# Kernel tuning notes

Measured on AMD Instinct MI355X. Metric: run time of the kernel, lower is better.

## Reference

```python
import jax, jax.numpy as jnp
import numpy as np

DIM = 1024
N_HEADS = 16
HEAD_DIM = DIM // N_HEADS
LN_EPS = 1e-5


def layer_norm(x, gamma, beta):
    mu = jnp.mean(x, axis=-1, keepdims=True)
    var = jnp.var(x, axis=-1, keepdims=True)
    return (x - mu) * jax.lax.rsqrt(var + LN_EPS) * gamma + beta


def setup_inputs() -> dict:
    key = jax.random.key(0)
    ks = jax.random.split(key, 12)
    B, Nq, Nc, D = 2, 2048, 2048, DIM
    s = 1.0 / np.sqrt(D)
    return {
        "query": jax.random.normal(ks[0], (B, Nq, D), jnp.float32),
        "context": jax.random.normal(ks[1], (B, Nc, D), jnp.float32),
        "Wq": jax.random.normal(ks[2], (D, D), jnp.float32) * s,
        "bq": jnp.zeros((D,), jnp.float32),
        "Wk": jax.random.normal(ks[3], (D, D), jnp.float32) * s,
        "bk": jnp.zeros((D,), jnp.float32),
        "Wv": jax.random.normal(ks[4], (D, D), jnp.float32) * s,
        "bv": jnp.zeros((D,), jnp.float32),
        "Wo": jax.random.normal(ks[5], (D, D), jnp.float32) * s,
        "bo": jnp.zeros((D,), jnp.float32),
        "gq": jnp.ones((D,), jnp.float32),
        "betaq": jnp.zeros((D,), jnp.float32),
        "gkv": jnp.ones((D,), jnp.float32),
        "betakv": jnp.zeros((D,), jnp.float32),
    }


def reference(query, context, Wq, bq, Wk, bk, Wv, bv, Wo, bo, gq, betaq, gkv, betakv):
    B, Nq, D = query.shape
    Nc = context.shape[1]
    residual = query
    q = layer_norm(query, gq, betaq)
    c = layer_norm(context, gkv, betakv)
    # projections; (B,N,D) -> (B,H,N,hd)
    Q = (q @ Wq + bq).reshape(B, Nq, N_HEADS, HEAD_DIM).transpose(0, 2, 1, 3)
    K = (c @ Wk + bk).reshape(B, Nc, N_HEADS, HEAD_DIM).transpose(0, 2, 1, 3)
    V = (c @ Wv + bv).reshape(B, Nc, N_HEADS, HEAD_DIM).transpose(0, 2, 1, 3)
    scores = jnp.einsum("bhqd,bhkd->bhqk", Q, K) / np.sqrt(HEAD_DIM).astype(np.float32)
    attn = jax.nn.softmax(scores, axis=-1)
    out = jnp.einsum("bhqk,bhkd->bhqd", attn, V)
    out = out.transpose(0, 2, 1, 3).reshape(B, Nq, D)
    return residual + out @ Wo + bo
```

## Files before the change

kernel.cpp:

```cpp
#include <hip/hip_runtime.h>
#include <hip/hip_bf16.h>

typedef unsigned short u16;
typedef unsigned long long u64;
typedef __bf16 bf16x8 __attribute__((ext_vector_type(8)));
typedef float f32x4 __attribute__((ext_vector_type(4)));

#define DIM 1024
#define NH 16
#define HD 64
#define QSCALE 0.180336880972788f

__device__ __forceinline__ u16 f2bf(float f) {
  union { float f; unsigned u; } v; v.f = f;
  unsigned r = v.u + 0x7fffu + ((v.u >> 16) & 1u);
  return (u16)(r >> 16);
}

__device__ __forceinline__ unsigned pk2(float a, float b) {
  union { __hip_bfloat162 h; unsigned u; } cv;
  cv.h = __float22bfloat162_rn(make_float2(a, b));
  return cv.u;
}

__device__ __forceinline__ float bf2f(unsigned s) {
  union { unsigned u; float f; } v; v.u = s << 16; return v.f;
}

__device__ __forceinline__ void gld16(const u16* gp, u16* lp) {
  __builtin_amdgcn_global_load_lds(
      (const __attribute__((address_space(1))) unsigned int*)(const void*)gp,
      (__attribute__((address_space(3))) unsigned int*)(void*)lp, 16, 0, 0);
}

__global__ __launch_bounds__(256) void prep_kernel(
    const float* __restrict__ q, const float* __restrict__ c,
    const float* __restrict__ gq, const float* __restrict__ bq,
    const float* __restrict__ gkv, const float* __restrict__ bkv,
    u16* __restrict__ qn, u16* __restrict__ cn,
    const float* W0, const float* W1, const float* W2, const float* W3,
    u16* O0, u16* O1, u16* O2, u16* O3) {
  __shared__ float red[2][4];
  __shared__ float t[32][33];
  int bid = blockIdx.x, tid = threadIdx.x;
  if (bid < 8192) {
    const float* x  = bid < 4096 ? q : c;
    const float* g  = bid < 4096 ? gq : gkv;
    const float* be = bid < 4096 ? bq : bkv;
    u16* out = bid < 4096 ? qn : cn;
    int row = bid & 4095;
    float4 v = ((const float4*)(x + (size_t)row * DIM))[tid];
    float s1 = v.x + v.y + v.z + v.w;
    float s2 = v.x * v.x + v.y * v.y + v.z * v.z + v.w * v.w;
#pragma unroll
    for (int o = 32; o >= 1; o >>= 1) { s1 += __shfl_xor(s1, o, 64); s2 += __shfl_xor(s2, o, 64); }
    int wv = tid >> 6;
    if ((tid & 63) == 0) { red[0][wv] = s1; red[1][wv] = s2; }
    __syncthreads();
    s1 = red[0][0] + red[0][1] + red[0][2] + red[0][3];
    s2 = red[1][0] + red[1][1] + red[1][2] + red[1][3];
    float mu = s1 * (1.f / DIM);
    float var = s2 * (1.f / DIM) - mu * mu;
    float rs = rsqrtf(var + 1e-5f);
    float4 gv = ((const float4*)g)[tid];
    float4 bv = ((const float4*)be)[tid];
    uint2 o2;
    o2.x = pk2((v.x - mu) * rs * gv.x + bv.x, (v.y - mu) * rs * gv.y + bv.y);
    o2.y = pk2((v.z - mu) * rs * gv.z + bv.z, (v.w - mu) * rs * gv.w + bv.w);
    ((uint2*)(out + (size_t)row * DIM))[tid] = o2;
  } else {
    int wid = bid - 8192;
    int z = wid >> 10;
    const float* W = z == 0 ? W0 : z == 1 ? W1 : z == 2 ? W2 : W3;
    u16* O        = z == 0 ? O0 : z == 1 ? O1 : z == 2 ? O2 : O3;
    int xy = wid & 1023;
    int bx = (xy & 31) * 32, by = (xy >> 5) * 32;
    int tx = tid & 31, ty = tid >> 5;
#pragma unroll
    for (int i = 0; i < 4; ++i) t[ty + i * 8][tx] = W[(size_t)(by + ty + i * 8) * DIM + bx + tx];
    __syncthreads();
#pragma unroll
    for (int i = 0; i < 4; ++i) O[(size_t)(bx + ty + i * 8) * DIM + by + tx] = f2bf(t[tx][ty + i * 8]);
  }
}

struct GArg { const u16* A; const u16* Bt; const float* bias; void* out; int mode; };
struct GArg3 { GArg g[3]; };

__global__ __launch_bounds__(256) void gemm128(GArg3 args) {
  GArg ga = args.g[blockIdx.z];
  const u16* __restrict__ A  = ga.A;
  const u16* __restrict__ Bt = ga.Bt;
  __shared__ __align__(16) u16 sm[128 * 64 * 2];
  u16* As = sm;
  u16* Bs = sm + 128 * 64;
  int tid = threadIdx.x, wave = tid >> 6, lane = tid & 63;
  int lr = lane & 15, quad = lane >> 4;
  int m0 = blockIdx.x * 128, n0 = blockIdx.y * 128;
  int wm = (wave >> 1) * 64, wn = (wave & 1) * 64;
  f32x4 acc[4][4] = {};
  for (int kt = 0; kt < DIM; kt += 64) {
#pragma unroll
    for (int r = 0; r < 4; ++r) {
      int slot = tid + r * 256;
      int row = slot >> 3;
      int c = (slot & 7) ^ (row & 7);
      gld16(A + (size_t)(m0 + row) * DIM + kt + c * 8, &As[slot * 8]);
    }
#pragma unroll
    for (int r = 0; r < 4; ++r) {
      int slot = tid + r * 256;
      int row = slot >> 3;
      int c = (slot & 7) ^ (row & 7);
      gld16(Bt + (size_t)(n0 + row) * DIM + kt + c * 8, &Bs[slot * 8]);
    }
    __syncthreads();
#pragma unroll
    for (int kc = 0; kc < 2; ++kc) {
      int pc = ((kc * 4 + quad) ^ (lr & 7)) * 8;
      bf16x8 af[4], bfr[4];
#pragma unroll
      for (int i = 0; i < 4; ++i) {
        af[i]  = *(const bf16x8*)&As[(wm + i * 16 + lr) * 64 + pc];
        bfr[i] = *(const bf16x8*)&Bs[(wn + i * 16 + lr) * 64 + pc];
      }
#pragma unroll
      for (int mi = 0; mi < 4; ++mi)
#pragma unroll
        for (int ni = 0; ni < 4; ++ni)
          acc[mi][ni] = __builtin_amdgcn_mfma_f32_16x16x32_bf16(af[mi], bfr[ni], acc[mi][ni], 0, 0, 0);
    }
    __syncthreads();
  }
  int mode = ga.mode;
  const float* bias = ga.bias;
#pragma unroll
  for (int mi = 0; mi < 4; ++mi)
#pragma unroll
    for (int ni = 0; ni < 4; ++ni) {
      int col = n0 + wn + ni * 16 + lr;
      float bv = bias[col];
      int row0 = m0 + wm + mi * 16 + quad * 4;
      if (mode == 2) {
        int bb = row0 >> 11, t0 = row0 & 2047;
        u64 pk = 0;
#pragma unroll
        for (int r = 0; r < 4; ++r)
          pk |= (u64)f2bf(acc[mi][ni][r] + bv) << (16 * r);
        *(u64*)&((u16*)ga.out)[((size_t)(bb << 10) + col) * 2048 + t0] = pk;
      } else {
        float sc = (mode == 1) ? QSCALE : 1.f;
#pragma unroll
        for (int r = 0; r < 4; ++r)
          ((u16*)ga.out)[(size_t)(row0 + r) * DIM + col] = f2bf((acc[mi][ni][r] + bv) * sc);
      }
    }
}

__global__ __launch_bounds__(256) void gemm_o(const u16* __restrict__ A,
    const u16* __restrict__ Bt, const float* __restrict__ bias,
    float* __restrict__ out, const float* __restrict__ resid) {
  __shared__ __align__(16) u16 sm[(128 + 64) * 64];
  u16* As = sm;
  u16* Bs = sm + 128 * 64;
  int tid = threadIdx.x, wave = tid >> 6, lane = tid & 63;
  int lr = lane & 15, quad = lane >> 4;
  int m0 = blockIdx.x * 128, n0 = blockIdx.y * 64;
  int wm = (wave >> 1) * 64, wn = (wave & 1) * 32;
  f32x4 acc[4][2] = {};
  for (int kt = 0; kt < DIM; kt += 64) {
#pragma unroll
    for (int r = 0; r < 4; ++r) {
      int slot = tid + r * 256;
      int row = slot >> 3;
      int c = (slot & 7) ^ (row & 7);
      gld16(A + (size_t)(m0 + row) * DIM + kt + c * 8, &As[slot * 8]);
    }
#pragma unroll
    for (int r = 0; r < 2; ++r) {
      int slot = tid + r * 256;
      int row = slot >> 3;
      int c = (slot & 7) ^ (row & 7);
      gld16(Bt + (size_t)(n0 + row) * DIM + kt + c * 8, &Bs[slot * 8]);
    }
    __syncthreads();
#pragma unroll
    for (int kc = 0; kc < 2; ++kc) {
      int pc = ((kc * 4 + quad) ^ (lr & 7)) * 8;
      bf16x8 af[4], bfr[2];
#pragma unroll
      for (int i = 0; i < 4; ++i) af[i] = *(const bf16x8*)&As[(wm + i * 16 + lr) * 64 + pc];
#pragma unroll
      for (int j = 0; j < 2; ++j) bfr[j] = *(const bf16x8*)&Bs[(wn + j * 16 + lr) * 64 + pc];
#pragma unroll
      for (int mi = 0; mi < 4; ++mi)
#pragma unroll
        for (int ni = 0; ni < 2; ++ni)
          acc[mi][ni] = __builtin_amdgcn_mfma_f32_16x16x32_bf16(af[mi], bfr[ni], acc[mi][ni], 0, 0, 0);
    }
    __syncthreads();
  }
#pragma unroll
  for (int mi = 0; mi < 4; ++mi)
#pragma unroll
    for (int ni = 0; ni < 2; ++ni) {
      int col = n0 + wn + ni * 16 + lr;
      float bv = bias[col];
      int row0 = m0 + wm + mi * 16 + quad * 4;
#pragma unroll
      for (int r = 0; r < 4; ++r) {
        int row = row0 + r;
        out[(size_t)row * DIM + col] = acc[mi][ni][r] + bv + resid[(size_t)row * DIM + col];
      }
    }
}

#define FK0 0
#define FV0 4096
#define FK1 8192
#define FV1 12288
#define FQP 16384
__global__ __launch_bounds__(256) void flash_kernel(const u16* __restrict__ Q,
    const u16* __restrict__ Kg, const u16* __restrict__ Vt,
    u16* __restrict__ O0, u16* __restrict__ O1,
    float* __restrict__ L0, float* __restrict__ L1) {
  __shared__ __align__(16) u16 lds[24576];
  int tid = threadIdx.x, wave = tid >> 6, lane = tid & 63;
  int lr = lane & 15, quad = lane >> 4;
  int bh = blockIdx.x, b = bh >> 4, h = bh & 15;
  int q0 = blockIdx.y * 128;
  int split = blockIdx.z;
  u16* Op = split ? O1 : O0;
  float* Lp = split ? L1 : L0;
  int t0 = split * 1024;

  const u16* qbase = Q + (size_t)(b * 2048 + q0) * DIM + h * HD;
  const u16* kbase = Kg + (size_t)(b * 2048 + t0) * DIM + h * HD;
  const u16* vbase = Vt + (size_t)(b * 1024 + h * HD) * 2048 + t0;

#pragma unroll
  for (int r = 0; r < 4; ++r) {
    int slot = tid + r * 256;
    int row = slot >> 3;
    int c = (slot & 7) ^ (row & 7);
    gld16(qbase + (size_t)row * DIM + c * 8, &lds[FQP + slot * 8]);
  }
#pragma unroll
  for (int r = 0; r < 2; ++r) {
    int slot = tid + r * 256;
    int row = slot >> 3;
    int c = (slot & 7) ^ (row & 7);
    gld16(kbase + (size_t)row * DIM + c * 8, &lds[FK0 + slot * 8]);
    gld16(vbase + (size_t)row * 2048 + c * 8, &lds[FV0 + slot * 8]);
  }
  __syncthreads();

  bf16x8 qf[2][2];
#pragma unroll
  for (int s = 0; s < 2; ++s)
#pragma unroll
    for (int kc = 0; kc < 2; ++kc)
      qf[s][kc] = *(const bf16x8*)&lds[FQP + (wave * 32 + s * 16 + lr) * 64 +
                                       (((kc * 4 + quad) ^ (lr & 7)) * 8)];

  int pb = FQP + wave * 2048;
  float plsum[2] = {0.f, 0.f};
  f32x4 oacc[2][4] = {};

  for (int j = 0; j < 16; ++j) {
    int cb = (j & 1) ? FK1 : FK0;
    if (j < 15) {
      int nb = (j & 1) ? FK0 : FK1;
      int nj = j * 64 + 64;
#pragma unroll
      for (int r = 0; r < 2; ++r) {
        int slot = tid + r * 256;
        int row = slot >> 3;
        int c = (slot & 7) ^ (row & 7);
        gld16(kbase + (size_t)(nj + row) * DIM + c * 8, &lds[nb + slot * 8]);
        gld16(vbase + (size_t)row * 2048 + nj + c * 8, &lds[nb + 4096 + slot * 8]);
      }
    }

    f32x4 sf[2][4] = {};
#pragma unroll
    for (int kc = 0; kc < 2; ++kc) {
      int pc = ((kc * 4 + quad) ^ (lr & 7)) * 8;
#pragma unroll
      for (int ns = 0; ns < 4; ++ns) {
        bf16x8 kf = *(const bf16x8*)&lds[cb + (ns * 16 + lr) * 64 + pc];
#pragma unroll
        for (int s = 0; s < 2; ++s)
          sf[s][ns] = __builtin_amdgcn_mfma_f32_16x16x32_bf16(kf, qf[s][kc], sf[s][ns], 0, 0, 0);
      }
    }

#pragma unroll
    for (int s = 0; s < 2; ++s)
#pragma unroll
      for (int ns = 0; ns < 4; ++ns) {
        float p0 = exp2f(sf[s][ns][0]), p1 = exp2f(sf[s][ns][1]);
        float p2 = exp2f(sf[s][ns][2]), p3 = exp2f(sf[s][ns][3]);
        plsum[s] += (p0 + p1) + (p2 + p3);
        uint2 pk;
        pk.x = pk2(p0, p1);
        pk.y = pk2(p2, p3);
        int chunk = ns * 2 + (quad >> 1);
        int off = pb + (s * 16 + lr) * 64 + ((chunk ^ (lr & 7)) * 8) + (quad & 1) * 4;
        *(uint2*)&lds[off] = pk;
      }
    __threadfence_block();

#pragma unroll
    for (int kc = 0; kc < 2; ++kc) {
      int pc = ((kc * 4 + quad) ^ (lr & 7)) * 8;
      bf16x8 pf[2];
#pragma unroll
      for (int s = 0; s < 2; ++s)
        pf[s] = *(const bf16x8*)&lds[pb + (s * 16 + lr) * 64 + pc];
#pragma unroll
      for (int ds = 0; ds < 4; ++ds) {
        bf16x8 vf = *(const bf16x8*)&lds[cb + 4096 + (ds * 16 + lr) * 64 + pc];
#pragma unroll
        for (int s = 0; s < 2; ++s)
          oacc[s][ds] = __builtin_amdgcn_mfma_f32_16x16x32_bf16(vf, pf[s], oacc[s][ds], 0, 0, 0);
      }
    }
    __syncthreads();
  }

#pragma unroll
  for (int s = 0; s < 2; ++s) {
    float l = plsum[s];
    l += __shfl_xor(l, 16, 64);
    l += __shfl_xor(l, 32, 64);
    size_t qrow = (size_t)(b * 2048 + q0 + wave * 32 + s * 16 + lr);
    if (quad == 0) Lp[qrow * 16 + h] = l;
#pragma unroll
    for (int ds = 0; ds < 4; ++ds) {
      uint2 pk;
      pk.x = pk2(oacc[s][ds][0], oacc[s][ds][1]);
      pk.y = pk2(oacc[s][ds][2], oacc[s][ds][3]);
      *(uint2*)&Op[qrow * DIM + h * HD + ds * 16 + quad * 4] = pk;
    }
  }
}

__global__ __launch_bounds__(256) void combine_kernel(const u16* __restrict__ O0,
    const u16* __restrict__ O1, const float* __restrict__ L0, const float* __restrict__ L1,
    u16* __restrict__ AO) {
  int row = blockIdx.x, tid = threadIdx.x;
  int h = tid >> 4;
  float rl = 1.f / (L0[row * 16 + h] + L1[row * 16 + h]);
  uint2 a = ((const uint2*)(O0 + (size_t)row * DIM))[tid];
  uint2 b = ((const uint2*)(O1 + (size_t)row * DIM))[tid];
  float v0 = (bf2f(a.x & 0xffff) + bf2f(b.x & 0xffff)) * rl;
  float v1 = (bf2f(a.x >> 16)    + bf2f(b.x >> 16))    * rl;
  float v2 = (bf2f(a.y & 0xffff) + bf2f(b.y & 0xffff)) * rl;
  float v3 = (bf2f(a.y >> 16)    + bf2f(b.y >> 16))    * rl;
  uint2 o;
  o.x = pk2(v0, v1);
  o.y = pk2(v2, v3);
  ((uint2*)(AO + (size_t)row * DIM))[tid] = o;
}

extern "C" void kernel_launch(void* const* d_in, const int* in_sizes, int n_in,
                              void* d_out, int out_size, void* d_ws, size_t ws_size,
                              hipStream_t stream) {
  const float* query   = (const float*)d_in[0];
  const float* context = (const float*)d_in[1];
  const float* Wq = (const float*)d_in[2];
  const float* bq = (const float*)d_in[3];
  const float* Wk = (const float*)d_in[4];
  const float* bk = (const float*)d_in[5];
  const float* Wv = (const float*)d_in[6];
  const float* bv = (const float*)d_in[7];
  const float* Wo = (const float*)d_in[8];
  const float* bo = (const float*)d_in[9];
  const float* gq    = (const float*)d_in[10];
  const float* betaq = (const float*)d_in[11];
  const float* gkv   = (const float*)d_in[12];
  const float* betakv= (const float*)d_in[13];
  (void)in_sizes; (void)n_in; (void)out_size; (void)ws_size;

  char* ws = (char*)d_ws;
  const size_t MB = (size_t)1 << 20;
  u16* qn  = (u16*)(ws + 0 * MB);
  u16* cn  = (u16*)(ws + 8 * MB);
  u16* Wqt = (u16*)(ws + 16 * MB);
  u16* Wkt = (u16*)(ws + 18 * MB);
  u16* Wvt = (u16*)(ws + 20 * MB);
  u16* Wot = (u16*)(ws + 22 * MB);
  u16* Qb  = (u16*)(ws + 24 * MB);
  u16* Kb  = (u16*)(ws + 32 * MB);
  u16* Vtb = (u16*)(ws + 40 * MB);
  u16* AOb = (u16*)(ws + 48 * MB);
  u16* Op0 = qn;
  u16* Op1 = cn;
  float* L0 = (float*)(ws + 16 * MB);
  float* L1 = (float*)(ws + 16 * MB + 256 * 1024);

  prep_kernel<<<12288, 256, 0, stream>>>(query, context, gq, betaq, gkv, betakv,
                                         qn, cn, Wq, Wk, Wv, Wo, Wqt, Wkt, Wvt, Wot);

  GArg3 a3;
  a3.g[0] = { qn, Wqt, bq, (void*)Qb,  1 };
  a3.g[1] = { cn, Wkt, bk, (void*)Kb,  0 };
  a3.g[2] = { cn, Wvt, bv, (void*)Vtb, 2 };
  gemm128<<<dim3(32, 8, 3), 256, 0, stream>>>(a3);

  flash_kernel<<<dim3(32, 16, 2), 256, 0, stream>>>(Qb, Kb, Vtb, Op0, Op1, L0, L1);

  combine_kernel<<<4096, 256, 0, stream>>>(Op0, Op1, L0, L1, AOb);

  gemm_o<<<dim3(32, 16), 256, 0, stream>>>(AOb, Wot, bo, (float*)d_out, query);
}
```

Measured before the change: 244.9 us.

## Rework V-projection store layout, flash Q loads, P staging and exp2

The V projection GEMM swaps MFMA operands so each lane writes transposed V with contiguous token indices instead of packed 64-bit stores. The flash kernel now loads Q fragments directly from global memory into registers rather than staging through LDS, which shrinks its LDS footprint. It also precomputes K/V pointers for the double-buffered prefetch, splits P staging into half-size per-kc chunks to interleave exp and PV MFMAs, and uses the hardware exp2 builtin. These touch several unrelated costs at once and risk less coalesced V stores and less coalesced Q loads.

```diff
diff --git a/kernel.cpp b/kernel.cpp
--- a/kernel.cpp
+++ b/kernel.cpp
@@ -25,6 +25,14 @@
 
 __device__ __forceinline__ float bf2f(unsigned s) {
   union { unsigned u; float f; } v; v.u = s << 16; return v.f;
+}
+
+__device__ __forceinline__ float fexp2(float x) {
+#if __has_builtin(__builtin_amdgcn_exp2f)
+  return __builtin_amdgcn_exp2f(x);
+#else
+  return exp2f(x);
+#endif
 }
 
 __device__ __forceinline__ void gld16(const u16* gp, u16* lp) {
@@ -98,6 +106,7 @@
   int lr = lane & 15, quad = lane >> 4;
   int m0 = blockIdx.x * 128, n0 = blockIdx.y * 128;
   int wm = (wave >> 1) * 64, wn = (wave & 1) * 64;
+  int mode = ga.mode;
   f32x4 acc[4][4] = {};
   for (int kt = 0; kt < DIM; kt += 64) {
 #pragma unroll
@@ -124,37 +133,51 @@
         af[i]  = *(const bf16x8*)&As[(wm + i * 16 + lr) * 64 + pc];
         bfr[i] = *(const bf16x8*)&Bs[(wn + i * 16 + lr) * 64 + pc];
       }
-#pragma unroll
-      for (int mi = 0; mi < 4; ++mi)
-#pragma unroll
-        for (int ni = 0; ni < 4; ++ni)
-          acc[mi][ni] = __builtin_amdgcn_mfma_f32_16x16x32_bf16(af[mi], bfr[ni], acc[mi][ni], 0, 0, 0);
-    }
-    __syncthreads();
-  }
-  int mode = ga.mode;
+      if (mode != 2) {
+#pragma unroll
+        for (int mi = 0; mi < 4; ++mi)
+#pragma unroll
+          for (int ni = 0; ni < 4; ++ni)
+            acc[mi][ni] = __builtin_amdgcn_mfma_f32_16x16x32_bf16(af[mi], bfr[ni], acc[mi][ni], 0, 0, 0);
+      } else {
+#pragma unroll
+        for (int mi = 0; mi < 4; ++mi)
+#pragma unroll
+          for (int ni = 0; ni < 4; ++ni)
+            acc[mi][ni] = __builtin_amdgcn_mfma_f32_16x16x32_bf16(bfr[ni], af[mi], acc[mi][ni], 0, 0, 0);
+      }
+    }
+    __syncthreads();
+  }
   const float* bias = ga.bias;
-#pragma unroll
-  for (int mi = 0; mi < 4; ++mi)
-#pragma unroll
-    for (int ni = 0; ni < 4; ++ni) {
-      int col = n0 + wn + ni * 16 + lr;
-      float bv = bias[col];
-      int row0 = m0 + wm + mi * 16 + quad * 4;
-      if (mode == 2) {
-        int bb = row0 >> 11, t0 = row0 & 2047;
-        u64 pk = 0;
+  if (mode == 2) {
+#pragma unroll
+    for (int mi = 0; mi < 4; ++mi) {
+      int m = m0 + wm + mi * 16 + lr;
+      int bb = m >> 11, tt = m & 2047;
+      u16* outb = (u16*)ga.out + (((size_t)bb << 10)) * 2048 + tt;
+#pragma unroll
+      for (int ni = 0; ni < 4; ++ni) {
+        int nbase = n0 + wn + ni * 16 + quad * 4;
 #pragma unroll
         for (int r = 0; r < 4; ++r)
-          pk |= (u64)f2bf(acc[mi][ni][r] + bv) << (16 * r);
-        *(u64*)&((u16*)ga.out)[((size_t)(bb << 10) + col) * 2048 + t0] = pk;
-      } else {
-        float sc = (mode == 1) ? QSCALE : 1.f;
+          outb[(size_t)(nbase + r) * 2048] = f2bf(acc[mi][ni][r] + bias[nbase + r]);
+      }
+    }
+  } else {
+    float sc = (mode == 1) ? QSCALE : 1.f;
+#pragma unroll
+    for (int mi = 0; mi < 4; ++mi)
+#pragma unroll
+      for (int ni = 0; ni < 4; ++ni) {
+        int col = n0 + wn + ni * 16 + lr;
+        float bv = bias[col];
+        int row0 = m0 + wm + mi * 16 + quad * 4;
 #pragma unroll
         for (int r = 0; r < 4; ++r)
           ((u16*)ga.out)[(size_t)(row0 + r) * DIM + col] = f2bf((acc[mi][ni][r] + bv) * sc);
       }
-    }
+  }
 }
 
 __global__ __launch_bounds__(256) void gemm_o(const u16* __restrict__ A,
@@ -215,16 +238,11 @@
     }
 }
 
-#define FK0 0
-#define FV0 4096
-#define FK1 8192
-#define FV1 12288
-#define FQP 16384
 __global__ __launch_bounds__(256) void flash_kernel(const u16* __restrict__ Q,
     const u16* __restrict__ Kg, const u16* __restrict__ Vt,
     u16* __restrict__ O0, u16* __restrict__ O1,
     float* __restrict__ L0, float* __restrict__ L1) {
-  __shared__ __align__(16) u16 lds[24576];
+  __shared__ __align__(16) u16 lds[20480];
   int tid = threadIdx.x, wave = tid >> 6, lane = tid & 63;
   int lr = lane & 15, quad = lane >> 4;
   int bh = blockIdx.x, b = bh >> 4, h = bh & 15;
@@ -234,52 +252,46 @@
   float* Lp = split ? L1 : L0;
   int t0 = split * 1024;
 
-  const u16* qbase = Q + (size_t)(b * 2048 + q0) * DIM + h * HD;
   const u16* kbase = Kg + (size_t)(b * 2048 + t0) * DIM + h * HD;
   const u16* vbase = Vt + (size_t)(b * 1024 + h * HD) * 2048 + t0;
 
-#pragma unroll
-  for (int r = 0; r < 4; ++r) {
-    int slot = tid + r * 256;
-    int row = slot >> 3;
-    int c = (slot & 7) ^ (row & 7);
-    gld16(qbase + (size_t)row * DIM + c * 8, &lds[FQP + slot * 8]);
-  }
-#pragma unroll
-  for (int r = 0; r < 2; ++r) {
-    int slot = tid + r * 256;
-    int row = slot >> 3;
-    int c = (slot & 7) ^ (row & 7);
-    gld16(kbase + (size_t)row * DIM + c * 8, &lds[FK0 + slot * 8]);
-    gld16(vbase + (size_t)row * 2048 + c * 8, &lds[FV0 + slot * 8]);
-  }
+  bf16x8 qf[2][2];
+#pragma unroll
+  for (int s = 0; s < 2; ++s)
+#pragma unroll
+    for (int kc = 0; kc < 2; ++kc)
+      qf[s][kc] = *(const bf16x8*)&Q[((size_t)(b * 2048 + q0 + wave * 32 + s * 16 + lr)) * DIM +
+                                     h * HD + kc * 32 + quad * 8];
+
+  int slot0 = tid, slot1 = tid + 256;
+  int r0 = slot0 >> 3, c0 = (slot0 & 7) ^ (r0 & 7);
+  int r1 = slot1 >> 3, c1 = (slot1 & 7) ^ (r1 & 7);
+  const u16* kp0 = kbase + (size_t)r0 * DIM + c0 * 8;
+  const u16* kp1 = kbase + (size_t)r1 * DIM + c1 * 8;
+  const u16* vp0 = vbase + (size_t)r0 * 2048 + c0 * 8;
+  const u16* vp1 = vbase + (size_t)r1 * 2048 + c1 * 8;
+
+  gld16(kp0, &lds[slot0 * 8]);
+  gld16(kp1, &lds[slot1 * 8]);
+  gld16(vp0, &lds[8192 + slot0 * 8]);
+  gld16(vp1, &lds[8192 + slot1 * 8]);
   __syncthreads();
 
-  bf16x8 qf[2][2];
-#pragma unroll
-  for (int s = 0; s < 2; ++s)
-#pragma unroll
-    for (int kc = 0; kc < 2; ++kc)
-      qf[s][kc] = *(const bf16x8*)&lds[FQP + (wave * 32 + s * 16 + lr) * 64 +
-                                       (((kc * 4 + quad) ^ (lr & 7)) * 8)];
-
-  int pb = FQP + wave * 2048;
+  u16* Pw = &lds[16384 + wave * 1024];
   float plsum[2] = {0.f, 0.f};
   f32x4 oacc[2][4] = {};
 
   for (int j = 0; j < 16; ++j) {
-    int cb = (j & 1) ? FK1 : FK0;
+    int par = j & 1;
+    const u16* kcb = &lds[par * 4096];
+    const u16* vcb = &lds[8192 + par * 4096];
     if (j < 15) {
-      int nb = (j & 1) ? FK0 : FK1;
-      int nj = j * 64 + 64;
-#pragma unroll
-      for (int r = 0; r < 2; ++r) {
-        int slot = tid + r * 256;
-        int row = slot >> 3;
-        int c = (slot & 7) ^ (row & 7);
-        gld16(kbase + (size_t)(nj + row) * DIM + c * 8, &lds[nb + slot * 8]);
-        gld16(vbase + (size_t)row * 2048 + nj + c * 8, &lds[nb + 4096 + slot * 8]);
-      }
+      int np = par ^ 1;
+      kp0 += 64 * DIM; kp1 += 64 * DIM; vp0 += 64; vp1 += 64;
+      gld16(kp0, &lds[np * 4096 + slot0 * 8]);
+      gld16(kp1, &lds[np * 4096 + slot1 * 8]);
+      gld16(vp0, &lds[8192 + np * 4096 + slot0 * 8]);
+      gld16(vp1, &lds[8192 + np * 4096 + slot1 * 8]);
     }
 
     f32x4 sf[2][4] = {};
@@ -288,7 +300,7 @@
       int pc = ((kc * 4 + quad) ^ (lr & 7)) * 8;
 #pragma unroll
       for (int ns = 0; ns < 4; ++ns) {
-        bf16x8 kf = *(const bf16x8*)&lds[cb + (ns * 16 + lr) * 64 + pc];
+        bf16x8 kf = *(const bf16x8*)&kcb[(ns * 16 + lr) * 64 + pc];
 #pragma unroll
         for (int s = 0; s < 2; ++s)
           sf[s][ns] = __builtin_amdgcn_mfma_f32_16x16x32_bf16(kf, qf[s][kc], sf[s][ns], 0, 0, 0);
@@ -296,31 +308,30 @@
     }
 
 #pragma unroll
-    for (int s = 0; s < 2; ++s)
-#pragma unroll
-      for (int ns = 0; ns < 4; ++ns) {
-        float p0 = exp2f(sf[s][ns][0]), p1 = exp2f(sf[s][ns][1]);
-        float p2 = exp2f(sf[s][ns][2]), p3 = exp2f(sf[s][ns][3]);
-        plsum[s] += (p0 + p1) + (p2 + p3);
-        uint2 pk;
-        pk.x = pk2(p0, p1);
-        pk.y = pk2(p2, p3);
-        int chunk = ns * 2 + (quad >> 1);
-        int off = pb + (s * 16 + lr) * 64 + ((chunk ^ (lr & 7)) * 8) + (quad & 1) * 4;
-        *(uint2*)&lds[off] = pk;
-      }
-    __threadfence_block();
-
-#pragma unroll
     for (int kc = 0; kc < 2; ++kc) {
-      int pc = ((kc * 4 + quad) ^ (lr & 7)) * 8;
+#pragma unroll
+      for (int s = 0; s < 2; ++s)
+#pragma unroll
+        for (int nsl = 0; nsl < 2; ++nsl) {
+          int ns = kc * 2 + nsl;
+          float p0 = fexp2(sf[s][ns][0]), p1 = fexp2(sf[s][ns][1]);
+          float p2 = fexp2(sf[s][ns][2]), p3 = fexp2(sf[s][ns][3]);
+          plsum[s] += (p0 + p1) + (p2 + p3);
+          uint2 pk;
+          pk.x = pk2(p0, p1);
+          pk.y = pk2(p2, p3);
+          int pp = (((nsl * 2 + (quad >> 1)) ^ (lr & 3)) * 8) + (quad & 1) * 4;
+          *(uint2*)&Pw[(s * 16 + lr) * 32 + pp] = pk;
+        }
+      __threadfence_block();
+      int pvc = ((kc * 4 + quad) ^ (lr & 7)) * 8;
       bf16x8 pf[2];
 #pragma unroll
       for (int s = 0; s < 2; ++s)
-        pf[s] = *(const bf16x8*)&lds[pb + (s * 16 + lr) * 64 + pc];
+        pf[s] = *(const bf16x8*)&Pw[(s * 16 + lr) * 32 + ((quad ^ (lr & 3)) * 8)];
 #pragma unroll
       for (int ds = 0; ds < 4; ++ds) {
-        bf16x8 vf = *(const bf16x8*)&lds[cb + 4096 + (ds * 16 + lr) * 64 + pc];
+        bf16x8 vf = *(const bf16x8*)&vcb[(ds * 16 + lr) * 64 + pvc];
 #pragma unroll
         for (int s = 0; s < 2; ++s)
           oacc[s][ds] = __builtin_amdgcn_mfma_f32_16x16x32_bf16(vf, pf[s], oacc[s][ds], 0, 0, 0);
```

Result: no change. 246.8 us (+0.8%).
